# Kernel optimization log

Measured on AMD Instinct MI355X. Metric: run time of the kernel, lower is better.

Reference implementation:

```python
import jax, jax.numpy as jnp
import numpy as np

B, N, C, H = 4, 2048, 256, 8
D = C // H  # head_dim = 32


def setup_inputs() -> dict:
    key = jax.random.key(0)
    ks = jax.random.split(key, 6)
    scale = 0.02
    return {
        "x": jax.random.normal(ks[0], (B, N, C), dtype=jnp.float32),
        # PPI interaction strengths in [0,1] (buffer, not trained)
        "interaction_mask": jax.random.uniform(ks[1], (N, N), dtype=jnp.float32),
        "W_qkv": jax.random.normal(ks[2], (C, 3 * C), dtype=jnp.float32) * scale,
        "b_qkv": jnp.zeros((3 * C,), dtype=jnp.float32),
        "W_out": jax.random.normal(ks[3], (C, C), dtype=jnp.float32) * scale,
        "b_out": jnp.zeros((C,), dtype=jnp.float32),
    }


def reference(x, interaction_mask, W_qkv, b_qkv, W_out, b_out):
    Bb, Nn, Cc = x.shape
    scale = D ** -0.5
    qkv = (x @ W_qkv + b_qkv).reshape(Bb, Nn, 3, H, D)
    qkv = jnp.transpose(qkv, (2, 0, 3, 1, 4))  # [3, B, H, N, D]
    q, k, v = qkv[0], qkv[1], qkv[2]
    # scores [B, H, N, N], modulated pre-softmax by biological mask
    attn = jnp.einsum("bhnd,bhmd->bhnm", q, k) * scale
    attn = attn * (0.1 + 0.9 * interaction_mask)[None, None, :, :]
    attn = jax.nn.softmax(attn, axis=-1)  # dropout is identity in eval
    out = jnp.einsum("bhnm,bhmd->bhnd", attn, v)
    out = jnp.transpose(out, (0, 2, 1, 3)).reshape(Bb, Nn, Cc)
    return out @ W_out + b_out
```

## Files before the change

### kernel.cpp

```cpp
#include <hip/hip_runtime.h>
#include <hip/hip_bf16.h>

#define B_ 4
#define N_ 2048
#define C_ 256
#define H_ 8
#define D_ 32

typedef __attribute__((ext_vector_type(4))) short bf16x4;
typedef __attribute__((ext_vector_type(8))) short bf16x8;
typedef __attribute__((ext_vector_type(16))) float f32x16;

static __device__ __forceinline__ float b2f(short u) {
    unsigned v = ((unsigned)(unsigned short)u) << 16;
    return __builtin_bit_cast(float, v);
}
static __device__ __forceinline__ short f2bs(float f) {
    __hip_bfloat16 h = __float2bfloat16(f);
    return __builtin_bit_cast(short, h);
}


__global__ __launch_bounds__(256) void prep_relayout(const float* __restrict__ x,
                                                     const float* __restrict__ Wq,
                                                     const float* __restrict__ Wo,
                                                     const float* __restrict__ mask,
                                                     short* __restrict__ xF,
                                                     short* __restrict__ wqF,
                                                     short* __restrict__ woF,
                                                     short* __restrict__ maskF) {
    const int t = threadIdx.x;
    const int b = blockIdx.x;
    if (b < 2048) {
        const int idx = b * 256 + t;
        const int row = idx >> 6, c0 = (idx & 63) * 4;
        const float4 f4 = *(const float4*)(x + (size_t)row * 256 + c0);
        const int mt = row >> 5, l5 = row & 31;
        const int kt = c0 >> 5, dd0 = c0 & 31;
        const int hi = (dd0 >> 2) & 1, s0 = 4 * (dd0 >> 3);
        bf16x4 o;
        o[0] = f2bs(f4.x); o[1] = f2bs(f4.y); o[2] = f2bs(f4.z); o[3] = f2bs(f4.w);
        *(bf16x4*)(xF + (((size_t)mt * 8 + kt) * 32 + l5) * 32 + hi * 16 + s0) = o;
    } else if (b < 2304) {
        int idx = (b - 2048) * 256 + t;
        const float* W; short* dst; int ncols;
        if (idx < 49152) { W = Wq; dst = wqF; ncols = 768; }
        else { idx -= 49152; W = Wo; dst = woF; ncols = 256; }
        const int f4pr = ncols >> 2;
        const int row = idx / f4pr, c0 = (idx % f4pr) * 4;
        const float4 f4 = *(const float4*)(W + (size_t)row * ncols + c0);
        const int kt = row >> 5, dd = row & 31;
        const int hi = (dd >> 2) & 1, s = (dd & 3) + 4 * (dd >> 3);
        const float vals[4] = {f4.x, f4.y, f4.z, f4.w};
#pragma unroll
        for (int j = 0; j < 4; ++j) {
            const int col = c0 + j, nt = col >> 5, l5 = col & 31;
            dst[(((size_t)nt * 8 + kt) * 32 + l5) * 32 + hi * 16 + s] = f2bs(vals[j]);
        }
    } else {
        const int bid = b - 2304;
        const int bx = bid & 15, by = bid >> 4;
        const int n = by * 64 + (t & 63);
        const int mt = bx * 4 + (t >> 6);
        const float cf = 0.17677669529663687f * 1.4426950408889634f;
        float v[32];
        const float4* src = (const float4*)(mask + (size_t)n * N_ + mt * 32);
#pragma unroll
        for (int i = 0; i < 8; ++i) {
            const float4 f4 = src[i];
            v[i * 4 + 0] = f4.x; v[i * 4 + 1] = f4.y;
            v[i * 4 + 2] = f4.z; v[i * 4 + 3] = f4.w;
        }
#pragma unroll
        for (int hi = 0; hi < 2; ++hi) {
            bf16x8 o0, o1;
#pragma unroll
            for (int r = 0; r < 16; ++r) {
                const int crow = (r & 3) + 8 * (r >> 2) + 4 * hi;
                const short s = f2bs(cf * (0.1f + 0.9f * v[crow]));
                if (r < 8) o0[r] = s; else o1[r - 8] = s;
            }
            short* dst = maskF + ((size_t)(mt * 2 + hi) * N_ + n) * 16;
            *(bf16x8*)dst = o0;
            *(bf16x8*)(dst + 8) = o1;
        }
    }
}

__global__ __launch_bounds__(256, 4) void qkv_mfma(const short* __restrict__ xF,
                                                   const short* __restrict__ wqF,
                                                   const float* __restrict__ bias,
                                                   short* __restrict__ qb,
                                                   short* __restrict__ kbF,
                                                   short* __restrict__ vbF) {
    __shared__ short sc[4][32 * 34];
    const int t = threadIdx.x;
    const int w = t >> 6, lane = t & 63, l5 = lane & 31, hi = lane >> 5;
    const int tile = blockIdx.x * 4 + w;
    const int nt = tile % 24, mt = tile / 24;
    f32x16 acc0, acc1;
#pragma unroll
    for (int i = 0; i < 16; ++i) { acc0[i] = 0.f; acc1[i] = 0.f; }
    const short* ap = xF + ((size_t)mt * 8 * 32) * 32 + l5 * 32 + hi * 16;
    const short* bp = wqF + ((size_t)nt * 8 * 32) * 32 + l5 * 32 + hi * 16;
#pragma unroll
    for (int kt = 0; kt < 8; kt += 2) {
        const bf16x8 a0 = *(const bf16x8*)(ap + kt * 1024);
        const bf16x8 a1 = *(const bf16x8*)(ap + kt * 1024 + 8);
        const bf16x8 b0 = *(const bf16x8*)(bp + kt * 1024);
        const bf16x8 b1 = *(const bf16x8*)(bp + kt * 1024 + 8);
        const bf16x8 a2 = *(const bf16x8*)(ap + kt * 1024 + 1024);
        const bf16x8 a3 = *(const bf16x8*)(ap + kt * 1024 + 1032);
        const bf16x8 b2 = *(const bf16x8*)(bp + kt * 1024 + 1024);
        const bf16x8 b3 = *(const bf16x8*)(bp + kt * 1024 + 1032);
        acc0 = __builtin_amdgcn_mfma_f32_32x32x16_bf16(a0, b0, acc0, 0, 0, 0);
        acc1 = __builtin_amdgcn_mfma_f32_32x32x16_bf16(a2, b2, acc1, 0, 0, 0);
        acc0 = __builtin_amdgcn_mfma_f32_32x32x16_bf16(a1, b1, acc0, 0, 0, 0);
        acc1 = __builtin_amdgcn_mfma_f32_32x32x16_bf16(a3, b3, acc1, 0, 0, 0);
    }
    const float bq = bias[nt * 32 + l5];
    short* myc = sc[w];
#pragma unroll
    for (int r = 0; r < 16; ++r)
        myc[((r & 3) + 8 * (r >> 2) + 4 * hi) * 34 + l5] =
            f2bs(acc0[r] + acc1[r] + bq);
    __syncthreads();

    const int h = nt & 7, t3 = nt >> 3;
    const int mtk = mt & 63;
    const size_t bh = (size_t)(mt >> 6) * 8 + h;
    if (t3 == 0) {
        const bf16x8 r0 = *(const bf16x8*)(myc + l5 * 34 + hi * 16);
        const bf16x8 r1 = *(const bf16x8*)(myc + l5 * 34 + hi * 16 + 8);
        short* dst = qb + (bh * N_ + (size_t)mtk * 32 + l5) * D_ + hi * 16;
        *(bf16x8*)dst = r0;
        *(bf16x8*)(dst + 8) = r1;
    } else if (t3 == 1) {
        bf16x8 o0, o1;
#pragma unroll
        for (int s = 0; s < 16; ++s) {
            const int dd = hi * 4 + (s & 3) + 8 * (s >> 2);
            const short vv = myc[l5 * 34 + dd];
            if (s < 8) o0[s] = vv; else o1[s - 8] = vv;
        }
        short* dst = kbF + ((bh * 64 + mtk) * 32 + l5) * 32 + hi * 16;
        *(bf16x8*)dst = o0;
        *(bf16x8*)(dst + 8) = o1;
    } else {
        bf16x8 o0, o1;
#pragma unroll
        for (int s = 0; s < 16; ++s) {
            const int nl = hi * 4 + (s & 3) + 8 * (s >> 2);
            const short vv = myc[nl * 34 + l5];
            if (s < 8) o0[s] = vv; else o1[s - 8] = vv;
        }
        short* dst = vbF + ((bh * 64 + mtk) * 32 + l5) * 32 + hi * 16;
        *(bf16x8*)dst = o0;
        *(bf16x8*)(dst + 8) = o1;
    }
}

__global__ __launch_bounds__(256, 4) void attn_mfma(const short* __restrict__ qb,
                                                    const short* __restrict__ kbF,
                                                    const short* __restrict__ vbF,
                                                    const short* __restrict__ maskF,
                                                    short* __restrict__ aoF) {
    __shared__ float red[4][32][33];
    __shared__ float Ls[4][32];
    const int t = threadIdx.x;
    const int w = t >> 6, lane = t & 63, l5 = lane & 31, hi = lane >> 5;
    const int hi4 = hi * 4;
    const int vb = (blockIdx.x & 7) * 128 + (blockIdx.x >> 3);
    const int bh = vb >> 5, qg = vb & 31;
    const int q0 = qg * 64;
    const int nqA = q0 + l5, nqB = q0 + 32 + l5;

    const short* qrA = qb + ((size_t)bh * N_ + nqA) * D_;
    const short* qrB = qb + ((size_t)bh * N_ + nqB) * D_;
    const bf16x8 qfA0 = __builtin_shufflevector(*(const bf16x4*)(qrA + hi4),
                                                *(const bf16x4*)(qrA + hi4 + 8),
                                                0, 1, 2, 3, 4, 5, 6, 7);
    const bf16x8 qfA1 = __builtin_shufflevector(*(const bf16x4*)(qrA + hi4 + 16),
                                                *(const bf16x4*)(qrA + hi4 + 24),
                                                0, 1, 2, 3, 4, 5, 6, 7);
    const bf16x8 qfB0 = __builtin_shufflevector(*(const bf16x4*)(qrB + hi4),
                                                *(const bf16x4*)(qrB + hi4 + 8),
                                                0, 1, 2, 3, 4, 5, 6, 7);
    const bf16x8 qfB1 = __builtin_shufflevector(*(const bf16x4*)(qrB + hi4 + 16),
                                                *(const bf16x4*)(qrB + hi4 + 24),
                                                0, 1, 2, 3, 4, 5, 6, 7);
    f32x16 accA, accB;
#pragma unroll
    for (int i = 0; i < 16; ++i) { accA[i] = 0.f; accB[i] = 0.f; }
    float lsA0 = 0.f, lsA1 = 0.f, lsB0 = 0.f, lsB1 = 0.f;

    const size_t fragbase = (size_t)bh * 64 * 1024;
#pragma unroll 4
    for (int i = 0; i < 16; ++i) {
        const int mt = w * 16 + i;
        const short* mpA = maskF + ((size_t)(mt * 2 + hi) * N_ + nqA) * 16;
        const short* mpB = maskF + ((size_t)(mt * 2 + hi) * N_ + nqB) * 16;
        const bf16x8 mA0 = *(const bf16x8*)mpA;
        const bf16x8 mA1 = *(const bf16x8*)(mpA + 8);
        const bf16x8 mB0 = *(const bf16x8*)mpB;
        const bf16x8 mB1 = *(const bf16x8*)(mpB + 8);
        const short* vp = vbF + fragbase + (size_t)mt * 1024 + l5 * 32 + hi * 16;
        const bf16x8 vf0 = *(const bf16x8*)vp;
        const bf16x8 vf1 = *(const bf16x8*)(vp + 8);

        const short* kp = kbF + fragbase + (size_t)mt * 1024 + l5 * 32 + hi * 16;
        const bf16x8 af0 = *(const bf16x8*)kp;
        const bf16x8 af1 = *(const bf16x8*)(kp + 8);
        f32x16 sA, sB;
#pragma unroll
        for (int j = 0; j < 16; ++j) { sA[j] = 0.f; sB[j] = 0.f; }
        __builtin_amdgcn_s_setprio(1);
        sA = __builtin_amdgcn_mfma_f32_32x32x16_bf16(af0, qfA0, sA, 0, 0, 0);
        sB = __builtin_amdgcn_mfma_f32_32x32x16_bf16(af0, qfB0, sB, 0, 0, 0);
        sA = __builtin_amdgcn_mfma_f32_32x32x16_bf16(af1, qfA1, sA, 0, 0, 0);
        sB = __builtin_amdgcn_mfma_f32_32x32x16_bf16(af1, qfB1, sB, 0, 0, 0);
        __builtin_amdgcn_s_setprio(0);

        bf16x8 pfA0, pfA1, pfB0, pfB1;
#pragma unroll
        for (int r = 0; r < 16; ++r) {
            const float fmA = b2f(r < 8 ? mA0[r] : mA1[r - 8]);
            const float fmB = b2f(r < 8 ? mB0[r] : mB1[r - 8]);
            const float pA = __builtin_amdgcn_exp2f(sA[r] * fmA);
            const float pB = __builtin_amdgcn_exp2f(sB[r] * fmB);
            if (r < 8) { lsA0 += pA; lsB0 += pB; }
            else       { lsA1 += pA; lsB1 += pB; }
            const short hA = f2bs(pA), hB = f2bs(pB);
            if (r < 8) { pfA0[r] = hA; pfB0[r] = hB; }
            else       { pfA1[r - 8] = hA; pfB1[r - 8] = hB; }
        }
        __builtin_amdgcn_s_setprio(1);
        accA = __builtin_amdgcn_mfma_f32_32x32x16_bf16(vf0, pfA0, accA, 0, 0, 0);
        accB = __builtin_amdgcn_mfma_f32_32x32x16_bf16(vf0, pfB0, accB, 0, 0, 0);
        accA = __builtin_amdgcn_mfma_f32_32x32x16_bf16(vf1, pfA1, accA, 0, 0, 0);
        accB = __builtin_amdgcn_mfma_f32_32x32x16_bf16(vf1, pfB1, accB, 0, 0, 0);
        __builtin_amdgcn_s_setprio(0);
    }
    const float lsA = lsA0 + lsA1, lsB = lsB0 + lsB1;

    const int h = bh & 7;
    const int gmtb = (bh >> 3) * 64 + qg * 2;
#pragma unroll
    for (int tq = 0; tq < 2; ++tq) {
        if (tq) __syncthreads();
        const float lsum = tq ? lsB : lsA;
        const f32x16 acc = tq ? accB : accA;
        const float lt = lsum + __shfl_xor(lsum, 32);
        Ls[w][l5] = lt;
#pragma unroll
        for (int r = 0; r < 16; ++r)
            red[w][(r & 3) + 8 * (r >> 2) + hi4][l5] = acc[r];
        __syncthreads();
        const int row = t & 31, hi2 = (t >> 5) & 1, sh = t >> 6;
        const float inv = 1.0f / (Ls[0][row] + Ls[1][row] + Ls[2][row] + Ls[3][row]);
        bf16x4 o;
#pragma unroll
        for (int j = 0; j < 4; ++j) {
            const int dd = hi2 * 4 + j + 8 * sh;
            o[j] = f2bs((red[0][dd][row] + red[1][dd][row] +
                         red[2][dd][row] + red[3][dd][row]) * inv);
        }
        const size_t gmt = gmtb + tq;
        *(bf16x4*)(aoF + ((gmt * 8 + h) * 32 + row) * 32 + hi2 * 16 + sh * 4) = o;
    }
}

__global__ __launch_bounds__(256, 4) void out_mfma(const short* __restrict__ aoF,
                                                   const short* __restrict__ woF,
                                                   const float* __restrict__ bias,
                                                   float* __restrict__ out) {
    const int t = threadIdx.x;
    const int w = t >> 6, lane = t & 63, l5 = lane & 31, hi = lane >> 5;
    const int tile = blockIdx.x * 4 + w;
    const int nt = tile & 7, mt = tile >> 3;
    f32x16 acc0, acc1;
#pragma unroll
    for (int i = 0; i < 16; ++i) { acc0[i] = 0.f; acc1[i] = 0.f; }
    const short* ap = aoF + (size_t)mt * 8192 + l5 * 32 + hi * 16;
    const short* bp = woF + (size_t)nt * 8192 + l5 * 32 + hi * 16;
#pragma unroll
    for (int kt = 0; kt < 8; kt += 2) {
        const bf16x8 a0 = *(const bf16x8*)(ap + kt * 1024);
        const bf16x8 a1 = *(const bf16x8*)(ap + kt * 1024 + 8);
        const bf16x8 b0 = *(const bf16x8*)(bp + kt * 1024);
        const bf16x8 b1 = *(const bf16x8*)(bp + kt * 1024 + 8);
        const bf16x8 a2 = *(const bf16x8*)(ap + kt * 1024 + 1024);
        const bf16x8 a3 = *(const bf16x8*)(ap + kt * 1024 + 1032);
        const bf16x8 b2 = *(const bf16x8*)(bp + kt * 1024 + 1024);
        const bf16x8 b3 = *(const bf16x8*)(bp + kt * 1024 + 1032);
        acc0 = __builtin_amdgcn_mfma_f32_32x32x16_bf16(a0, b0, acc0, 0, 0, 0);
        acc1 = __builtin_amdgcn_mfma_f32_32x32x16_bf16(a2, b2, acc1, 0, 0, 0);
        acc0 = __builtin_amdgcn_mfma_f32_32x32x16_bf16(a1, b1, acc0, 0, 0, 0);
        acc1 = __builtin_amdgcn_mfma_f32_32x32x16_bf16(a3, b3, acc1, 0, 0, 0);
    }
    const float bo = bias[nt * 32 + l5];
#pragma unroll
    for (int r = 0; r < 16; ++r) {
        const int crow = (r & 3) + 8 * (r >> 2) + 4 * hi;
        out[(size_t)(mt * 32 + crow) * 256 + nt * 32 + l5] =
            acc0[r] + acc1[r] + bo;
    }
}

extern "C" void kernel_launch(void* const* d_in, const int* in_sizes, int n_in,
                              void* d_out, int out_size, void* d_ws, size_t ws_size,
                              hipStream_t stream) {
    const float* x = (const float*)d_in[0];
    const float* mask = (const float*)d_in[1];
    const float* W_qkv = (const float*)d_in[2];
    const float* b_qkv = (const float*)d_in[3];
    const float* W_out = (const float*)d_in[4];
    const float* b_out = (const float*)d_in[5];
    float* out = (float*)d_out;

    const size_t per = (size_t)B_ * H_ * N_ * D_;
    short* qb = (short*)d_ws;
    short* kbF = qb + per;
    short* vbF = kbF + per;
    short* maskF = vbF + per;
    short* xF = maskF + (size_t)N_ * N_;
    short* wqF = xF + per;
    short* woF = wqF + 196608;
    short* aoF = xF;

    prep_relayout<<<2816, 256, 0, stream>>>(x, W_qkv, W_out, mask,
                                            xF, wqF, woF, maskF);
    qkv_mfma<<<1536, 256, 0, stream>>>(xF, wqF, b_qkv, qb, kbF, vbF);
    attn_mfma<<<1024, 256, 0, stream>>>(qb, kbF, vbF, maskF, aoF);
    out_mfma<<<512, 256, 0, stream>>>(aoF, woF, b_out, out);
}
```

Baseline: 83.20 us.

## Quantize interaction mask to uint8 and apply affine transform in attention

The preprocessed mask is stored as 8-bit unsigned integers instead of bf16 scale factors, and the attention kernel rebuilds the 0.1+0.9*m scale with an fma per element. This halves the bytes of the mask workspace written in prep and read repeatedly by every batch-head block in the attention kernel. The attention block index swizzle is replaced by a plain mapping, and the setprio hints around the MFMA groups are dropped. Quantizing to 256 levels adds mask error on top of the earlier bf16 rounding and adds integer unpack and convert instructions in the inner loop.

```diff
diff --git a/kernel.cpp b/kernel.cpp
--- a/kernel.cpp
+++ b/kernel.cpp
@@ -11,13 +11,12 @@
 typedef __attribute__((ext_vector_type(8))) short bf16x8;
 typedef __attribute__((ext_vector_type(16))) float f32x16;
 
-static __device__ __forceinline__ float b2f(short u) {
-    unsigned v = ((unsigned)(unsigned short)u) << 16;
-    return __builtin_bit_cast(float, v);
-}
 static __device__ __forceinline__ short f2bs(float f) {
     __hip_bfloat16 h = __float2bfloat16(f);
     return __builtin_bit_cast(short, h);
+}
+static __device__ __forceinline__ float ub2f(unsigned dw, int b) {
+    return (float)((dw >> (8 * b)) & 0xffu);
 }
 
 
@@ -28,7 +27,7 @@
                                                      short* __restrict__ xF,
                                                      short* __restrict__ wqF,
                                                      short* __restrict__ woF,
-                                                     short* __restrict__ maskF) {
+                                                     unsigned char* __restrict__ maskU) {
     const int t = threadIdx.x;
     const int b = blockIdx.x;
     if (b < 2048) {
@@ -62,7 +61,6 @@
         const int bx = bid & 15, by = bid >> 4;
         const int n = by * 64 + (t & 63);
         const int mt = bx * 4 + (t >> 6);
-        const float cf = 0.17677669529663687f * 1.4426950408889634f;
         float v[32];
         const float4* src = (const float4*)(mask + (size_t)n * N_ + mt * 32);
 #pragma unroll
@@ -73,16 +71,16 @@
         }
 #pragma unroll
         for (int hi = 0; hi < 2; ++hi) {
-            bf16x8 o0, o1;
+            unsigned dw[4] = {0, 0, 0, 0};
 #pragma unroll
             for (int r = 0; r < 16; ++r) {
                 const int crow = (r & 3) + 8 * (r >> 2) + 4 * hi;
-                const short s = f2bs(cf * (0.1f + 0.9f * v[crow]));
-                if (r < 8) o0[r] = s; else o1[r - 8] = s;
+                const unsigned q =
+                    (unsigned)(int)rintf(fminf(fmaxf(v[crow], 0.f), 1.f) * 255.f);
+                dw[r >> 2] |= q << (8 * (r & 3));
             }
-            short* dst = maskF + ((size_t)(mt * 2 + hi) * N_ + n) * 16;
-            *(bf16x8*)dst = o0;
-            *(bf16x8*)(dst + 8) = o1;
+            uint4 o4 = {dw[0], dw[1], dw[2], dw[3]};
+            *(uint4*)(maskU + ((size_t)(mt * 2 + hi) * N_ + n) * 16) = o4;
         }
     }
 }
@@ -163,17 +161,18 @@
 __global__ __launch_bounds__(256, 4) void attn_mfma(const short* __restrict__ qb,
                                                     const short* __restrict__ kbF,
                                                     const short* __restrict__ vbF,
-                                                    const short* __restrict__ maskF,
+                                                    const unsigned char* __restrict__ maskU,
                                                     short* __restrict__ aoF) {
     __shared__ float red[4][32][33];
     __shared__ float Ls[4][32];
     const int t = threadIdx.x;
     const int w = t >> 6, lane = t & 63, l5 = lane & 31, hi = lane >> 5;
     const int hi4 = hi * 4;
-    const int vb = (blockIdx.x & 7) * 128 + (blockIdx.x >> 3);
-    const int bh = vb >> 5, qg = vb & 31;
+    const int bh = blockIdx.x >> 5, qg = blockIdx.x & 31;
     const int q0 = qg * 64;
     const int nqA = q0 + l5, nqB = q0 + 32 + l5;
+    const float c1 = 0.17677669529663687f * 1.4426950408889634f * 0.9f / 255.f;
+    const float c0 = 0.17677669529663687f * 1.4426950408889634f * 0.1f;
 
     const short* qrA = qb + ((size_t)bh * N_ + nqA) * D_;
     const short* qrB = qb + ((size_t)bh * N_ + nqB) * D_;
@@ -198,12 +197,8 @@
 #pragma unroll 4
     for (int i = 0; i < 16; ++i) {
         const int mt = w * 16 + i;
-        const short* mpA = maskF + ((size_t)(mt * 2 + hi) * N_ + nqA) * 16;
-        const short* mpB = maskF + ((size_t)(mt * 2 + hi) * N_ + nqB) * 16;
-        const bf16x8 mA0 = *(const bf16x8*)mpA;
-        const bf16x8 mA1 = *(const bf16x8*)(mpA + 8);
-        const bf16x8 mB0 = *(const bf16x8*)mpB;
-        const bf16x8 mB1 = *(const bf16x8*)(mpB + 8);
+        const uint4 muA = *(const uint4*)(maskU + ((size_t)(mt * 2 + hi) * N_ + nqA) * 16);
+        const uint4 muB = *(const uint4*)(maskU + ((size_t)(mt * 2 + hi) * N_ + nqB) * 16);
         const short* vp = vbF + fragbase + (size_t)mt * 1024 + l5 * 32 + hi * 16;
         const bf16x8 vf0 = *(const bf16x8*)vp;
         const bf16x8 vf1 = *(const bf16x8*)(vp + 8);
@@ -214,18 +209,20 @@
         f32x16 sA, sB;
 #pragma unroll
         for (int j = 0; j < 16; ++j) { sA[j] = 0.f; sB[j] = 0.f; }
-        __builtin_amdgcn_s_setprio(1);
         sA = __builtin_amdgcn_mfma_f32_32x32x16_bf16(af0, qfA0, sA, 0, 0, 0);
         sB = __builtin_amdgcn_mfma_f32_32x32x16_bf16(af0, qfB0, sB, 0, 0, 0);
         sA = __builtin_amdgcn_mfma_f32_32x32x16_bf16(af1, qfA1, sA, 0, 0, 0);
         sB = __builtin_amdgcn_mfma_f32_32x32x16_bf16(af1, qfB1, sB, 0, 0, 0);
-        __builtin_amdgcn_s_setprio(0);
 
         bf16x8 pfA0, pfA1, pfB0, pfB1;
 #pragma unroll
         for (int r = 0; r < 16; ++r) {
-            const float fmA = b2f(r < 8 ? mA0[r] : mA1[r - 8]);
-            const float fmB = b2f(r < 8 ? mB0[r] : mB1[r - 8]);
+            const unsigned dwA = (r < 4) ? muA.x : (r < 8) ? muA.y
+                               : (r < 12) ? muA.z : muA.w;
+            const unsigned dwB = (r < 4) ? muB.x : (r < 8) ? muB.y
+                               : (r < 12) ? muB.z : muB.w;
+            const float fmA = fmaf(ub2f(dwA, r & 3), c1, c0);
+            const float fmB = fmaf(ub2f(dwB, r & 3), c1, c0);
             const float pA = __builtin_amdgcn_exp2f(sA[r] * fmA);
             const float pB = __builtin_amdgcn_exp2f(sB[r] * fmB);
             if (r < 8) { lsA0 += pA; lsB0 += pB; }
@@ -234,12 +231,10 @@
             if (r < 8) { pfA0[r] = hA; pfB0[r] = hB; }
             else       { pfA1[r - 8] = hA; pfB1[r - 8] = hB; }
         }
-        __builtin_amdgcn_s_setprio(1);
         accA = __builtin_amdgcn_mfma_f32_32x32x16_bf16(vf0, pfA0, accA, 0, 0, 0);
         accB = __builtin_amdgcn_mfma_f32_32x32x16_bf16(vf0, pfB0, accB, 0, 0, 0);
         accA = __builtin_amdgcn_mfma_f32_32x32x16_bf16(vf1, pfA1, accA, 0, 0, 0);
         accB = __builtin_amdgcn_mfma_f32_32x32x16_bf16(vf1, pfB1, accB, 0, 0, 0);
-        __builtin_amdgcn_s_setprio(0);
     }
     const float lsA = lsA0 + lsA1, lsB = lsB0 + lsB1;
 
@@ -322,15 +317,15 @@
     short* qb = (short*)d_ws;
     short* kbF = qb + per;
     short* vbF = kbF + per;
-    short* maskF = vbF + per;
-    short* xF = maskF + (size_t)N_ * N_;
+    unsigned char* maskU = (unsigned char*)(vbF + per);
+    short* xF = (short*)(maskU + (size_t)N_ * N_);
     short* wqF = xF + per;
     short* woF = wqF + 196608;
     short* aoF = xF;
 
     prep_relayout<<<2816, 256, 0, stream>>>(x, W_qkv, W_out, mask,
-                                            xF, wqF, woF, maskF);
+                                            xF, wqF, woF, maskU);
     qkv_mfma<<<1536, 256, 0, stream>>>(xF, wqF, b_qkv, qb, kbF, vbF);
-    attn_mfma<<<1024, 256, 0, stream>>>(qb, kbF, vbF, maskF, aoF);
+    attn_mfma<<<1024, 256, 0, stream>>>(qb, kbF, vbF, maskU, aoF);
     out_mfma<<<512, 256, 0, stream>>>(aoF, woF, b_out, out);
 }
```

New measurement: 87.88 us. 5.6% more time.
